# Kernel tuning notes

Measured on AMD Instinct MI355X. Metric: run time of the kernel, lower is better.

The kernel has to match this reference:

```python
import jax, jax.numpy as jnp
import numpy as np

HEADS = 8
DIM_HEAD = 64


def setup_inputs() -> dict:
    key = jax.random.key(0)
    k1, k2, k3 = jax.random.split(key, 3)
    dim = 512
    hidden = HEADS * DIM_HEAD  # 512
    x = jax.random.normal(k1, (16, dim, 64, 64), dtype=jnp.float32)
    # 1x1 convs expressed as dense matrices (out_ch, in_ch)
    w_qkv = jax.random.normal(k2, (3 * hidden, dim), dtype=jnp.float32) * (1.0 / np.sqrt(dim))
    w_out = jax.random.normal(k3, (dim, hidden), dtype=jnp.float32) * (1.0 / np.sqrt(hidden))
    b_out = jnp.zeros((dim,), dtype=jnp.float32)
    return {"x": x, "w_qkv": w_qkv, "w_out": w_out, "b_out": b_out}


def reference(x, w_qkv, w_out, b_out):
    b, c, h, w = x.shape
    hw = h * w
    # 1x1 conv == channel matmul: (b, 3*hidden, hw)
    xf = x.reshape(b, c, hw)
    qkv = jnp.einsum('oc,bcn->bon', w_qkv, xf)
    # split into q,k,v each (b, heads, dim_head, hw)
    qkv = qkv.reshape(b, 3, HEADS, DIM_HEAD, hw)
    q, k, v = qkv[:, 0], qkv[:, 1], qkv[:, 2]
    k = jax.nn.softmax(k, axis=-1)  # softmax over spatial dim
    # context: (b, heads, dim_head, dim_head)
    context = jnp.einsum('bhcn,bhdn->bhcd', k, v)
    # out: context^T @ q -> (b, heads, dim_head, hw)
    out = jnp.einsum('bhcd,bhcn->bhdn', context, q)
    out = out.reshape(b, HEADS * DIM_HEAD, h, w)
    # to_out 1x1 conv with bias
    outf = out.reshape(b, HEADS * DIM_HEAD, hw)
    y = jnp.einsum('oc,bcn->bon', w_out, outf) + b_out[None, :, None]
    return y.reshape(b, -1, h, w)
```

## Files before the change

### kernel.cpp

```cpp
#include <hip/hip_runtime.h>
#include <string.h>

typedef __bf16 bf16x8 __attribute__((ext_vector_type(8)));
typedef float f32x4 __attribute__((ext_vector_type(4)));
typedef unsigned short u16;
typedef u16 u16x8 __attribute__((ext_vector_type(8)));

#define NB 16
#define CD 512
#define NN 4096
#define O3 1536

__device__ __forceinline__ u16 f2bf(float f) {
    union { float f; unsigned int u; } v; v.f = f;
    unsigned int r = v.u + 0x7fffu + ((v.u >> 16) & 1u);
    return (u16)(r >> 16);
}
__device__ __forceinline__ float bf2f(u16 s) {
    union { unsigned int u; float f; } v; v.u = ((unsigned int)s) << 16;
    return v.f;
}

__device__ __forceinline__ void gl2lds16(const u16* g, u16* l) {
    __builtin_amdgcn_global_load_lds(
        (const void __attribute__((address_space(1)))*)g,
        (void __attribute__((address_space(3)))*)l,
        16, 0, 0);
}

__global__ void k_convert(const float* __restrict__ in, u16* __restrict__ out, int n) {
    int i = blockIdx.x * 256 + threadIdx.x;
    if (i < n) out[i] = f2bf(in[i]);
}

__global__ __launch_bounds__(256) void k_transpose_x(const float* __restrict__ x,
                                                     u16* __restrict__ xt) {
    __shared__ float tile[64][65];
    const int b = blockIdx.y;
    const int ntile = blockIdx.x & 63;
    const int ctile = blockIdx.x >> 6;
    const int t = threadIdx.x;
    const int r = t >> 2;
    const int q = t & 3;

    const float* xb = x + ((size_t)b * CD + ctile * 64 + r) * NN + ntile * 64;
#pragma unroll
    for (int j = 0; j < 4; ++j) {
        float4 v = *(const float4*)&xb[q * 16 + j * 4];
        tile[r][q * 16 + j * 4 + 0] = v.x;
        tile[r][q * 16 + j * 4 + 1] = v.y;
        tile[r][q * 16 + j * 4 + 2] = v.z;
        tile[r][q * 16 + j * 4 + 3] = v.w;
    }
    __syncthreads();
    u16* xtb = xt + ((size_t)b * NN + ntile * 64 + r) * CD + ctile * 64 + q * 16;
    u16x8 o0, o1;
#pragma unroll
    for (int j = 0; j < 8; ++j) {
        o0[j] = f2bf(tile[q * 16 + j][r]);
        o1[j] = f2bf(tile[q * 16 + 8 + j][r]);
    }
    *(u16x8*)&xtb[0] = o0;
    *(u16x8*)&xtb[8] = o1;
}


__device__ __forceinline__ void lda8(const u16* p, bf16x8 (&aa)[4][2],
                                     int aoff, int sw0, int sw1) {
#pragma unroll
    for (int mi = 0; mi < 4; ++mi) {
        aa[mi][0] = *(const bf16x8*)&p[aoff + mi * 1024 + sw0];
        aa[mi][1] = *(const bf16x8*)&p[aoff + mi * 1024 + sw1];
    }
}

__device__ __forceinline__ void ldb4(const u16* p, bf16x8 (&bb)[2][2],
                                     int boff, int sw0, int sw1) {
#pragma unroll
    for (int ni = 0; ni < 2; ++ni) {
        bb[ni][0] = *(const bf16x8*)&p[boff + ni * 1024 + sw0];
        bb[ni][1] = *(const bf16x8*)&p[boff + ni * 1024 + sw1];
    }
}

__device__ __forceinline__ void mfma16(bf16x8 (&aa)[4][2], bf16x8 (&bb)[2][2],
                                       f32x4 (&ac)[4][2]) {
    __builtin_amdgcn_s_setprio(1);
#pragma unroll
    for (int mi = 0; mi < 4; ++mi)
#pragma unroll
        for (int ni = 0; ni < 2; ++ni) {
            ac[mi][ni] = __builtin_amdgcn_mfma_f32_16x16x32_bf16(
                aa[mi][0], bb[ni][0], ac[mi][ni], 0, 0, 0);
            ac[mi][ni] = __builtin_amdgcn_mfma_f32_16x16x32_bf16(
                aa[mi][1], bb[ni][1], ac[mi][ni], 0, 0, 0);
        }
    __builtin_amdgcn_s_setprio(0);
}

#define MIDBAR() do { \
    asm volatile("" ::: "memory"); \
    __builtin_amdgcn_s_barrier(); \
    asm volatile("s_waitcnt lgkmcnt(0)" ::: "memory"); \
} while (0)

#define ENDBAR() do { \
    asm volatile("" ::: "memory"); \
    __builtin_amdgcn_s_barrier(); \
    asm volatile("" ::: "memory"); \
} while (0)

__device__ __forceinline__ void gemm256_core(const u16* __restrict__ Abase,
                                             const u16* __restrict__ Bbase,
                                             f32x4 (&acc)[2][2][4][2]) {
    __shared__ __align__(16) u16 lds[2][2][2][8192];

    const int t = threadIdx.x;
    const int lane = t & 63;
    const int w = t >> 6;
    const int l15 = lane & 15, quad = lane >> 4;
    const int r0 = t >> 3;
    const int sg = ((t & 7) ^ (r0 & 7)) * 8;
    const int aoff = ((w >> 2) * 64 + l15) * 64;
    const int boff = ((w & 3) * 32 + l15) * 64;
    const int sw0 = ((0 + quad) ^ (l15 & 7)) * 8;
    const int sw1 = ((4 + quad) ^ (l15 & 7)) * 8;

    auto stage = [&](int op, int half, int tau) {
        const u16* s = (op ? Bbase : Abase)
                       + (size_t)(half * 128 + r0) * CD + tau * 64 + sg;
        u16* d = &lds[tau & 1][op][half][t * 8];
        gl2lds16(s, d);
        gl2lds16(s + (size_t)64 * CD, d + 4096);
    };

    stage(0, 0, 0); stage(1, 0, 0); stage(1, 1, 0); stage(0, 1, 0);
    stage(0, 0, 1); stage(1, 0, 1);
    asm volatile("s_waitcnt vmcnt(4)" ::: "memory");
    ENDBAR();

    bf16x8 aa[4][2], bb0[2][2], bb1[2][2];
    for (int kt = 0; kt < 8; ++kt) {
        const int s = kt & 1;
        lda8(&lds[s][0][0][0], aa, aoff, sw0, sw1);
        ldb4(&lds[s][1][0][0], bb0, boff, sw0, sw1);
        if (kt <= 6) stage(1, 1, kt + 1);
        MIDBAR();
        mfma16(aa, bb0, acc[0][0]);
        ENDBAR();
        ldb4(&lds[s][1][1][0], bb1, boff, sw0, sw1);
        if (kt <= 6) stage(0, 1, kt + 1);
        MIDBAR();
        mfma16(aa, bb1, acc[0][1]);
        ENDBAR();
        lda8(&lds[s][0][1][0], aa, aoff, sw0, sw1);
        if (kt <= 5) stage(0, 0, kt + 2);
        MIDBAR();
        mfma16(aa, bb0, acc[1][0]);
        ENDBAR();
        if (kt <= 5) stage(1, 0, kt + 2);
        MIDBAR();
        mfma16(aa, bb1, acc[1][1]);
        if (kt == 6)      asm volatile("s_waitcnt vmcnt(0)" ::: "memory");
        else if (kt < 6)  asm volatile("s_waitcnt vmcnt(4)" ::: "memory");
        ENDBAR();
    }
}

__global__ __launch_bounds__(512, 2) void k_gemm1(
        const u16* __restrict__ A, const u16* __restrict__ Bt,
        u16* __restrict__ qt, u16* __restrict__ kbuf, u16* __restrict__ vbuf) {
    const int gid = blockIdx.x;
    const int u = (gid & 7) * 192 + (gid >> 3);
    const int mt = u % 6;
    const int bn = u / 6;
    const int b = bn >> 4;
    const int nt = bn & 15;
    const int t = threadIdx.x;
    const int lane = t & 63, w = t >> 6;
    const int l15 = lane & 15, quad = lane >> 4;

    f32x4 acc[2][2][4][2] = {};
    gemm256_core(A + (size_t)(mt * 256) * CD,
                 Bt + ((size_t)b * NN + nt * 256) * CD, acc);

    const int sec = mt >> 1;
    const int lrb = mt * 256 - sec * 512;
#pragma unroll
    for (int qm = 0; qm < 2; ++qm)
#pragma unroll
    for (int mi = 0; mi < 4; ++mi) {
        const int ml = qm * 128 + (w >> 2) * 64 + mi * 16 + quad * 4;
#pragma unroll
        for (int qn = 0; qn < 2; ++qn)
#pragma unroll
        for (int ni = 0; ni < 2; ++ni) {
            const int n = nt * 256 + qn * 128 + (w & 3) * 32 + ni * 16 + l15;
            f32x4 v = acc[qm][qn][mi][ni];
            if (sec == 0) {
                ushort4 pk;
                pk.x = f2bf(v[0]); pk.y = f2bf(v[1]);
                pk.z = f2bf(v[2]); pk.w = f2bf(v[3]);
                *(ushort4*)&qt[((size_t)b * NN + n) * CD + mt * 256 + ml] = pk;
            } else {
                u16* dst = (sec == 1) ? kbuf : vbuf;
#pragma unroll
                for (int r = 0; r < 4; ++r)
                    dst[((size_t)(b * 512 + lrb + ml + r)) * NN + n] = f2bf(v[r]);
            }
        }
    }
}

__global__ __launch_bounds__(256) void k_ctx(const u16* __restrict__ kbuf,
                                             const u16* __restrict__ vbuf,
                                             float* __restrict__ ctxT,
                                             float* __restrict__ lsum) {
    const int bh = blockIdx.y;
    const int chunk = blockIdx.x;
    const int t = threadIdx.x, lane = t & 63, w = t >> 6;
    const int l15 = lane & 15, quad = lane >> 4;
    const int cb = w * 16;

    const u16* krow = kbuf + (size_t)(bh * 64 + cb + l15) * NN;
    const u16* vb   = vbuf + (size_t)bh * 64 * NN;

    f32x4 acc[4] = {};
    float ls = 0.f;
    for (int i = 0; i < 32; ++i) {
        int n0 = chunk * 1024 + i * 32 + quad * 8;
        u16x8 ku = *(const u16x8*)&krow[n0];
        u16x8 afu;
#pragma unroll
        for (int jj = 0; jj < 8; ++jj) {
            float ev = __expf(fminf(bf2f(ku[jj]), 30.f));
            ls += ev;
            afu[jj] = f2bf(ev);
        }
        bf16x8 af = __builtin_bit_cast(bf16x8, afu);
#pragma unroll
        for (int di = 0; di < 4; ++di) {
            bf16x8 bfv = *(const bf16x8*)&vb[(size_t)(di * 16 + l15) * NN + n0];
            acc[di] = __builtin_amdgcn_mfma_f32_16x16x32_bf16(af, bfv, acc[di], 0, 0, 0);
        }
    }
    ls += __shfl_xor(ls, 16);
    ls += __shfl_xor(ls, 32);
    if (quad == 0) atomicAdd(&lsum[(size_t)bh * 64 + cb + l15], ls);

    const int c = cb + quad * 4;
#pragma unroll
    for (int di = 0; di < 4; ++di) {
        int d = di * 16 + l15;
#pragma unroll
        for (int r = 0; r < 4; ++r)
            atomicAdd(&ctxT[((size_t)bh * 64 + d) * 64 + c + r], acc[di][r]);
    }
}

__global__ __launch_bounds__(256) void k_weff(const float* __restrict__ wout,
                                              const float* __restrict__ ctxT,
                                              const float* __restrict__ lsum,
                                              u16* __restrict__ weff) {
    int idx = blockIdx.x * 256 + threadIdx.x;
    int b = idx >> 18;
    int o = (idx >> 9) & 511;
    int hc = idx & 511;
    int h = hc >> 6, c = hc & 63;
    const float* wr = wout + o * 512 + h * 64;
    const float* cr = ctxT + ((size_t)b * 8 + h) * 4096 + c;
    float s = 0.f;
#pragma unroll
    for (int d = 0; d < 64; ++d) s += wr[d] * cr[d * 64];
    s *= 1.0f / lsum[((size_t)b * 8 + h) * 64 + c];
    weff[idx] = f2bf(s);
}

__global__ __launch_bounds__(512, 2) void k_gemm2(
        const u16* __restrict__ weff, const u16* __restrict__ qt,
        const float* __restrict__ bout, float* __restrict__ y) {
    const int gid = blockIdx.x;
    const int u = (gid & 7) * 64 + (gid >> 3);
    const int mt = u & 1;
    const int bn = u >> 1;
    const int b = bn >> 4;
    const int nt = bn & 15;
    const int t = threadIdx.x;
    const int lane = t & 63, w = t >> 6;
    const int l15 = lane & 15, quad = lane >> 4;

    f32x4 acc[2][2][4][2] = {};
    gemm256_core(weff + (size_t)b * 512 * 512 + (size_t)(mt * 256) * CD,
                 qt + ((size_t)b * NN + nt * 256) * CD, acc);

#pragma unroll
    for (int qm = 0; qm < 2; ++qm)
#pragma unroll
    for (int mi = 0; mi < 4; ++mi) {
        const int o = mt * 256 + qm * 128 + (w >> 2) * 64 + mi * 16 + quad * 4;
#pragma unroll
        for (int qn = 0; qn < 2; ++qn)
#pragma unroll
        for (int ni = 0; ni < 2; ++ni) {
            const int n = nt * 256 + qn * 128 + (w & 3) * 32 + ni * 16 + l15;
            f32x4 v = acc[qm][qn][mi][ni];
#pragma unroll
            for (int r = 0; r < 4; ++r)
                y[((size_t)(b * 512 + o + r)) * NN + n] = v[r] + bout[o + r];
        }
    }
}

extern "C" void kernel_launch(void* const* d_in, const int* in_sizes, int n_in,
                              void* d_out, int out_size, void* d_ws, size_t ws_size,
                              hipStream_t stream) {
    const float* x    = (const float*)d_in[0];
    const float* wqkv = (const float*)d_in[1];
    const float* wout = (const float*)d_in[2];
    const float* bout = (const float*)d_in[3];
    float* y = (float*)d_out;

    char* ws = (char*)d_ws;
    u16*   xt   = (u16*)(ws);
    u16*   wqb  = (u16*)(ws + 67108864);
    u16*   qt   = (u16*)(ws + 68681728);
    u16*   kbuf = (u16*)(ws + 135790592);
    u16*   vbuf = (u16*)(ws + 202899456);
    float* ctxT = (float*)(ws + 270008320);
    float* lsum = (float*)(ws + 272105472);
    u16*   weff = (u16*)(ws + 272138240);

    hipMemsetAsync(ctxT, 0, 2097152 + 32768, stream);

    k_convert<<<(O3 * CD + 255) / 256, 256, 0, stream>>>(wqkv, wqb, O3 * CD);
    k_transpose_x<<<dim3(64 * 8, NB), 256, 0, stream>>>(x, xt);
    k_gemm1<<<1536, 512, 0, stream>>>(wqb, xt, qt, kbuf, vbuf);
    k_ctx<<<dim3(4, NB * 8), 256, 0, stream>>>(kbuf, vbuf, ctxT, lsum);
    k_weff<<<(NB * 512 * 512) / 256, 256, 0, stream>>>(wout, ctxT, lsum, weff);
    k_gemm2<<<512, 512, 0, stream>>>(weff, qt, bout, y);
}
```

Measured before the change: 523.8 us.

## Restructure GEMM main loop to halve barriers and prefetch next B fragment

Reorders the 256x256 GEMM k-loop so each iteration uses four barriers instead of eight and drops the explicit lgkmcnt waits. The next tile's first B fragment is loaded from LDS before the iteration ends, and both half-tile stages for kt+1 are issued together. LDS is moved from a function-static array into a per-kernel shared buffer passed by pointer. The aim is to cut barrier stalls and overlap LDS reads with MFMA work. The risk is races on double-buffered LDS, since the reads now rely on compiler-inserted waits and the reduced barrier set.

```diff
diff --git a/kernel.cpp b/kernel.cpp
--- a/kernel.cpp
+++ b/kernel.cpp
@@ -98,23 +98,16 @@
     __builtin_amdgcn_s_setprio(0);
 }
 
-#define MIDBAR() do { \
-    asm volatile("" ::: "memory"); \
-    __builtin_amdgcn_s_barrier(); \
-    asm volatile("s_waitcnt lgkmcnt(0)" ::: "memory"); \
-} while (0)
-
-#define ENDBAR() do { \
+#define BAR() do { \
     asm volatile("" ::: "memory"); \
     __builtin_amdgcn_s_barrier(); \
     asm volatile("" ::: "memory"); \
 } while (0)
 
-__device__ __forceinline__ void gemm256_core(const u16* __restrict__ Abase,
+__device__ __forceinline__ void gemm256_core(u16* __restrict__ smem,
+                                             const u16* __restrict__ Abase,
                                              const u16* __restrict__ Bbase,
                                              f32x4 (&acc)[2][2][4][2]) {
-    __shared__ __align__(16) u16 lds[2][2][2][8192];
-
     const int t = threadIdx.x;
     const int lane = t & 63;
     const int w = t >> 6;
@@ -126,10 +119,14 @@
     const int sw0 = ((0 + quad) ^ (l15 & 7)) * 8;
     const int sw1 = ((4 + quad) ^ (l15 & 7)) * 8;
 
+    auto ldsAt = [&](int s, int op, int half) -> u16* {
+        return smem + (size_t)(((s * 2 + op) * 2 + half) * 8192);
+    };
+
     auto stage = [&](int op, int half, int tau) {
         const u16* s = (op ? Bbase : Abase)
                        + (size_t)(half * 128 + r0) * CD + tau * 64 + sg;
-        u16* d = &lds[tau & 1][op][half][t * 8];
+        u16* d = ldsAt(tau & 1, op, half) + t * 8;
         gl2lds16(s, d);
         gl2lds16(s + (size_t)64 * CD, d + 4096);
     };
@@ -137,39 +134,37 @@
     stage(0, 0, 0); stage(1, 0, 0); stage(1, 1, 0); stage(0, 1, 0);
     stage(0, 0, 1); stage(1, 0, 1);
     asm volatile("s_waitcnt vmcnt(4)" ::: "memory");
-    ENDBAR();
+    BAR();
 
     bf16x8 aa[4][2], bb0[2][2], bb1[2][2];
+    ldb4(ldsAt(0, 1, 0), bb0, boff, sw0, sw1);
+
     for (int kt = 0; kt < 8; ++kt) {
         const int s = kt & 1;
-        lda8(&lds[s][0][0][0], aa, aoff, sw0, sw1);
-        ldb4(&lds[s][1][0][0], bb0, boff, sw0, sw1);
-        if (kt <= 6) stage(1, 1, kt + 1);
-        MIDBAR();
+        lda8(ldsAt(s, 0, 0), aa, aoff, sw0, sw1);
+        ldb4(ldsAt(s, 1, 1), bb1, boff, sw0, sw1);
+        if (kt <= 6) { stage(1, 1, kt + 1); stage(0, 1, kt + 1); }
         mfma16(aa, bb0, acc[0][0]);
-        ENDBAR();
-        ldb4(&lds[s][1][1][0], bb1, boff, sw0, sw1);
-        if (kt <= 6) stage(0, 1, kt + 1);
-        MIDBAR();
+        BAR();
+        if (kt <= 5) stage(0, 0, kt + 2);
         mfma16(aa, bb1, acc[0][1]);
-        ENDBAR();
-        lda8(&lds[s][0][1][0], aa, aoff, sw0, sw1);
-        if (kt <= 5) stage(0, 0, kt + 2);
-        MIDBAR();
+        BAR();
+        lda8(ldsAt(s, 0, 1), aa, aoff, sw0, sw1);
+        if (kt <= 5) stage(1, 0, kt + 2);
         mfma16(aa, bb0, acc[1][0]);
-        ENDBAR();
-        if (kt <= 5) stage(1, 0, kt + 2);
-        MIDBAR();
+        if (kt <= 5)      asm volatile("s_waitcnt vmcnt(4)" ::: "memory");
+        else if (kt == 6) asm volatile("s_waitcnt vmcnt(0)" ::: "memory");
+        BAR();
+        if (kt <= 6) ldb4(ldsAt(s ^ 1, 1, 0), bb0, boff, sw0, sw1);
         mfma16(aa, bb1, acc[1][1]);
-        if (kt == 6)      asm volatile("s_waitcnt vmcnt(0)" ::: "memory");
-        else if (kt < 6)  asm volatile("s_waitcnt vmcnt(4)" ::: "memory");
-        ENDBAR();
+        BAR();
     }
 }
 
 __global__ __launch_bounds__(512, 2) void k_gemm1(
         const u16* __restrict__ A, const u16* __restrict__ Bt,
         u16* __restrict__ qt, u16* __restrict__ kbuf, u16* __restrict__ vbuf) {
+    __shared__ __align__(16) u16 smem[65536];
     const int gid = blockIdx.x;
     const int u = (gid & 7) * 192 + (gid >> 3);
     const int mt = u % 6;
@@ -181,7 +176,7 @@
     const int l15 = lane & 15, quad = lane >> 4;
 
     f32x4 acc[2][2][4][2] = {};
-    gemm256_core(A + (size_t)(mt * 256) * CD,
+    gemm256_core(smem, A + (size_t)(mt * 256) * CD,
                  Bt + ((size_t)b * NN + nt * 256) * CD, acc);
 
     const int sec = mt >> 1;
@@ -279,6 +274,7 @@
 __global__ __launch_bounds__(512, 2) void k_gemm2(
         const u16* __restrict__ weff, const u16* __restrict__ qt,
         const float* __restrict__ bout, float* __restrict__ y) {
+    __shared__ __align__(16) u16 smem[65536];
     const int gid = blockIdx.x;
     const int u = (gid & 7) * 64 + (gid >> 3);
     const int mt = u & 1;
@@ -290,7 +286,7 @@
     const int l15 = lane & 15, quad = lane >> 4;
 
     f32x4 acc[2][2][4][2] = {};
-    gemm256_core(weff + (size_t)b * 512 * 512 + (size_t)(mt * 256) * CD,
+    gemm256_core(smem, weff + (size_t)b * 512 * 512 + (size_t)(mt * 256) * CD,
                  qt + ((size_t)b * NN + nt * 256) * CD, acc);
 
 #pragma unroll
```

After: 517.3 us. No clear change (-1.2%).
